# Kernel tuning notes

Hardware: AMD Instinct MI355X
Metric: run time of the kernel (lower is better)

The kernel has to match this reference:

```python
import jax, jax.numpy as jnp
import numpy as np

N_NODES = 50000


def setup_inputs() -> dict:
    key = jax.random.key(0)
    k1, k2, k3, k4 = jax.random.split(key, 4)
    x = jax.random.normal(k1, (N_NODES, 128), dtype=jnp.float32)
    edge_index = jax.random.randint(k2, (2, 1600000), 0, N_NODES, dtype=jnp.int64)
    W1 = jax.random.normal(k3, (128, 256), dtype=jnp.float32) * (1.0 / np.sqrt(128))
    b1 = jnp.zeros((256,), dtype=jnp.float32)
    W2 = jax.random.normal(k4, (256, 1), dtype=jnp.float32) * (1.0 / np.sqrt(256))
    b2 = jnp.zeros((1,), dtype=jnp.float32)
    return {"x": x, "edge_index": edge_index, "W1": W1, "b1": b1, "W2": W2, "b2": b2}


def _gcn_conv(x, src, dst, norm, W, b, n_nodes):
    # PyG GCNConv: h = X W; out_i = sum_j norm_ij * h_j (+ self loop) + b
    h = x @ W                               # [N, F_out]
    msg = h[src] * norm[:, None]            # [E', F_out] gather + scale
    out = jax.ops.segment_sum(msg, dst, num_segments=n_nodes)  # scatter-add
    return out + b


def reference(x, edge_index, W1, b1, W2, b2):
    n = x.shape[0]
    loop = jnp.arange(n, dtype=edge_index.dtype)
    src = jnp.concatenate([edge_index[0], loop])   # add self loops
    dst = jnp.concatenate([edge_index[1], loop])
    # symmetric degree normalization on A + I
    deg = jax.ops.segment_sum(jnp.ones_like(dst, dtype=x.dtype), dst, num_segments=n)
    dis = jnp.where(deg > 0, jax.lax.rsqrt(deg), 0.0)
    norm = dis[src] * dis[dst]                     # [E']
    h = jax.nn.relu(_gcn_conv(x, src, dst, norm, W1, b1, n))
    return _gcn_conv(h, src, dst, norm, W2, b2, n)
```

## Files before the change

kernel.cpp:

```cpp
#include <hip/hip_runtime.h>


#define EPB_LOG 12
#define EPB (1 << EPB_LOG)
#define BW_LOG 7
#define BW (1 << BW_LOG)
#define MAXBUCK 512
#define SCAN_TILE 2048
#define AMSTRIDE 136

typedef __attribute__((ext_vector_type(8))) short bf16x8;
typedef __attribute__((ext_vector_type(4))) float f32x4;

__device__ inline unsigned short f2bf(float f) {
    unsigned int b = __float_as_uint(f);
    unsigned int r = b + 0x7FFFu + ((b >> 16) & 1u);
    return (unsigned short)(r >> 16);
}
__device__ inline float bf_lo(unsigned int u) { return __uint_as_float(u << 16); }
__device__ inline float bf_hi(unsigned int u) { return __uint_as_float(u & 0xFFFF0000u); }

__device__ inline int detect_stride(const int* edges, int t, int* sh) {
    if (t < 64) {
        int v = edges[2 * t + 1];
        unsigned long long bb = __ballot(v != 0);
        if (t == 0) *sh = bb ? 1 : 2;
    }
    __syncthreads();
    return *sh;
}


__global__ __launch_bounds__(256) void k_count(
        const int* __restrict__ edges, const float* __restrict__ W1,
        unsigned short* __restrict__ w1t, int* __restrict__ btot_raw,
        long long E, int nbuck, int nsb) {
    int b = blockIdx.x, t = threadIdx.x;
    if (b >= nsb) {
        int row = (b - nsb) * 2 + (t >> 7);
        int k = t & 127;
        w1t[row * 128 + k] = f2bf(W1[k * 256 + row]);
        return;
    }
    __shared__ int bins[MAXBUCK];
    __shared__ int sh;
    for (int i = t; i < nbuck; i += 256) bins[i] = 0;
    int stride = detect_stride(edges, t, &sh);
    long long base = (long long)b << EPB_LOG;
    long long rem = E - base;
    int nE = (rem < (long long)EPB) ? (int)rem : EPB;
    for (int i = t; i < nE; i += 256) {
        int d = edges[(E + base + i) * stride];
        atomicAdd(&bins[d >> BW_LOG], 1);
    }
    __syncthreads();
    for (int i = t; i < nbuck; i += 256)
        if (bins[i]) atomicAdd(&btot_raw[i], bins[i]);
}

__global__ __launch_bounds__(256) void k_btot_scan(
        const int* __restrict__ btot_raw, int* __restrict__ btot,
        int* __restrict__ curg, int nbuck) {
    __shared__ int ws4[4];
    int t = threadIdx.x;
    int c4 = (nbuck + 255) >> 8;
    int lo = t * c4;
    int hi = lo + c4; if (hi > nbuck) hi = nbuck;
    if (lo > nbuck) lo = nbuck;
    int vals[2];
    int local = 0;
    for (int i = lo; i < hi; ++i) { vals[i - lo] = btot_raw[i]; local += vals[i - lo]; }
    int lane = t & 63, w = t >> 6;
    int inc = local;
    for (int off = 1; off < 64; off <<= 1) {
        int u = __shfl_up(inc, off, 64);
        if (lane >= off) inc += u;
    }
    if (lane == 63) ws4[w] = inc;
    __syncthreads();
    int woff = 0;
    for (int i = 0; i < w; ++i) woff += ws4[i];
    int ex = woff + inc - local;
    for (int i = lo; i < hi; ++i) {
        btot[i] = ex; curg[i] = ex;
        ex += vals[i - lo];
    }
}

__global__ __launch_bounds__(256) void k_partition(
        const int* __restrict__ edges, int* __restrict__ curg,
        unsigned int* __restrict__ part, long long E, int nbuck) {
    __shared__ unsigned int stage[EPB];
    __shared__ unsigned short dst16[EPB];
    __shared__ int bins[MAXBUCK];
    __shared__ int lcur[MAXBUCK];
    __shared__ int gbase[MAXBUCK];
    __shared__ int ws4[4];
    __shared__ int sh;
    int sb = blockIdx.x, t = threadIdx.x;
    for (int i = t; i < nbuck; i += 256) bins[i] = 0;
    int stride = detect_stride(edges, t, &sh);
    long long base = (long long)sb << EPB_LOG;
    long long rem = E - base;
    int nE = (rem < (long long)EPB) ? (int)rem : EPB;
    for (int i = t; i < nE; i += 256) {
        int d = edges[(E + base + i) * stride];
        dst16[i] = (unsigned short)d;
        atomicAdd(&bins[d >> BW_LOG], 1);
    }
    __syncthreads();
    int c4 = (nbuck + 255) >> 8;
    int lo = t * c4;
    int hi = lo + c4; if (hi > nbuck) hi = nbuck;
    if (lo > nbuck) lo = nbuck;
    int vals[2];
    int local = 0;
    for (int i = lo; i < hi; ++i) { vals[i - lo] = bins[i]; local += vals[i - lo]; }
    for (int i = t; i < nbuck; i += 256) {
        int c = bins[i];
        gbase[i] = c ? atomicAdd(&curg[i], c) : 0;
    }
    __syncthreads();
    int lane = t & 63, w = t >> 6;
    int inc = local;
    for (int off = 1; off < 64; off <<= 1) {
        int u = __shfl_up(inc, off, 64);
        if (lane >= off) inc += u;
    }
    if (lane == 63) ws4[w] = inc;
    __syncthreads();
    int woff = 0;
    for (int i = 0; i < w; ++i) woff += ws4[i];
    int ex = woff + inc - local;
    for (int i = lo; i < hi; ++i) {
        bins[i] = ex;
        lcur[i] = ex;
        ex += vals[i - lo];
    }
    __syncthreads();
    for (int i = t; i < nE; i += 256) {
        int s = edges[(base + i) * stride];
        int d = dst16[i];
        int b = d >> BW_LOG;
        int p = atomicAdd(&lcur[b], 1);
        stage[p] = ((unsigned int)s << 16) | (unsigned int)d;
    }
    __syncthreads();
    for (int i = t; i < nE; i += 256) {
        unsigned int pk = stage[i];
        int b = (int)(pk & 0xFFFFu) >> BW_LOG;
        part[gbase[b] + (i - bins[b])] = pk;
    }
}

__global__ __launch_bounds__(256) void k_build_csr(
        const unsigned int* __restrict__ part, const int* __restrict__ btot,
        const float* __restrict__ x, int* __restrict__ row_start,
        float* __restrict__ dis, int* __restrict__ csr_src,
        unsigned short* __restrict__ xs, int nbuck, int n, long long E) {
    __shared__ int c128[BW];
    __shared__ int lcur[BW];
    __shared__ float dld[BW];
    __shared__ int ws2[2];
    int b = blockIdx.x, t = threadIdx.x;
    if (t < BW) c128[t] = 0;
    __syncthreads();
    int start = btot[b];
    int endp = (b + 1 < nbuck) ? btot[b + 1] : (int)E;
    for (int i = start + t; i < endp; i += 256)
        atomicAdd(&c128[part[i] & (BW - 1)], 1);
    __syncthreads();
    int lane = t & 63, w = t >> 6;
    int deg = (t < BW) ? c128[t] : 0;
    int inc = deg;
    for (int off = 1; off < 64; off <<= 1) {
        int u = __shfl_up(inc, off, 64);
        if (lane >= off) inc += u;
    }
    if (t < BW && lane == 63) ws2[w] = inc;
    __syncthreads();
    if (t < BW) {
        int ex = inc - deg + ((w == 1) ? ws2[0] : 0);
        lcur[t] = ex;
        int d = (b << BW_LOG) + t;
        if (d < n) {
            row_start[d] = start + ex;
            float dv = rsqrtf((float)deg + 1.0f);
            dis[d] = dv;
            dld[t] = dv;
        }
    }
    if (b == nbuck - 1 && t == 0) row_start[n] = (int)E;
    __syncthreads();
    for (int i = start + t; i < endp; i += 256) {
        unsigned int pk = part[i];
        int r = atomicAdd(&lcur[pk & (BW - 1)], 1);
        csr_src[start + r] = (int)(pk >> 16);
    }
    int d0 = b << BW_LOG;
    for (int idx = t; idx < BW * 32; idx += 256) {
        int node = d0 + (idx >> 5);
        if (node >= n) break;
        float dv = dld[idx >> 5];
        float4 v = ((const float4*)x)[(size_t)node * 32 + (idx & 31)];
        ushort4 o;
        o.x = f2bf(v.x * dv); o.y = f2bf(v.y * dv);
        o.z = f2bf(v.z * dv); o.w = f2bf(v.w * dv);
        ((ushort4*)xs)[(size_t)node * 32 + (idx & 31)] = o;
    }
}

__global__ __launch_bounds__(512) void k_agg_mm(
        const unsigned short* __restrict__ xs, const int* __restrict__ csr_src,
        const int* __restrict__ rs, const float* __restrict__ dis,
        const unsigned short* __restrict__ w1t, const float* __restrict__ b1,
        const float* __restrict__ W2, float* __restrict__ svs, int n) {
    __shared__ short am[64 * AMSTRIDE];
    int t = threadIdx.x;
    int lane = t & 63, w = t >> 6;
    int blk = blockIdx.x;
    const unsigned int* xsu = (const unsigned int*)xs;
#pragma unroll 1
    for (int jj = 0; jj < 8; ++jj) {
        int r = w * 8 + jj;
        int node = blk * 64 + r;
        unsigned int pack = 0;
        if (node < n) {
            int start = rs[node], end = rs[node + 1];
            unsigned int self = xsu[((size_t)node << 6) + lane];
            float a0 = bf_lo(self), a1 = bf_hi(self);
            int e = start;
            for (; e + 7 < end; e += 8) {
                int s0 = csr_src[e],     s1 = csr_src[e + 1];
                int s2 = csr_src[e + 2], s3 = csr_src[e + 3];
                int s4 = csr_src[e + 4], s5 = csr_src[e + 5];
                int s6 = csr_src[e + 6], s7 = csr_src[e + 7];
                unsigned int v0 = xsu[((size_t)s0 << 6) + lane];
                unsigned int v1 = xsu[((size_t)s1 << 6) + lane];
                unsigned int v2 = xsu[((size_t)s2 << 6) + lane];
                unsigned int v3 = xsu[((size_t)s3 << 6) + lane];
                unsigned int v4 = xsu[((size_t)s4 << 6) + lane];
                unsigned int v5 = xsu[((size_t)s5 << 6) + lane];
                unsigned int v6 = xsu[((size_t)s6 << 6) + lane];
                unsigned int v7 = xsu[((size_t)s7 << 6) + lane];
                a0 += bf_lo(v0); a1 += bf_hi(v0);
                a0 += bf_lo(v1); a1 += bf_hi(v1);
                a0 += bf_lo(v2); a1 += bf_hi(v2);
                a0 += bf_lo(v3); a1 += bf_hi(v3);
                a0 += bf_lo(v4); a1 += bf_hi(v4);
                a0 += bf_lo(v5); a1 += bf_hi(v5);
                a0 += bf_lo(v6); a1 += bf_hi(v6);
                a0 += bf_lo(v7); a1 += bf_hi(v7);
            }
            for (; e < end; ++e) {
                int s0 = csr_src[e];
                unsigned int v0 = xsu[((size_t)s0 << 6) + lane];
                a0 += bf_lo(v0); a1 += bf_hi(v0);
            }
            float dn = dis[node];
            pack = (unsigned int)f2bf(a0 * dn) | ((unsigned int)f2bf(a1 * dn) << 16);
        }
        *(unsigned int*)&am[r * AMSTRIDE + 2 * lane] = pack;
    }
    __syncthreads();
    if (w >= 4) return;
    int m = lane & 15;
    int quad = lane >> 4;
    int node0 = blk * 64 + w * 16;

    bf16x8 afrag[4];
    const short* arow = &am[(w * 16 + m) * AMSTRIDE + quad * 8];
#pragma unroll
    for (int ks = 0; ks < 4; ++ks)
        afrag[ks] = *(const bf16x8*)(arow + ks * 32);

    float p0 = 0.f, p1 = 0.f, p2 = 0.f, p3 = 0.f;
#pragma unroll 1
    for (int tt = 0; tt < 16; ++tt) {
        const unsigned short* brow = w1t + (size_t)(tt * 16 + m) * 128 + quad * 8;
        f32x4 acc = {0.f, 0.f, 0.f, 0.f};
#pragma unroll
        for (int ks = 0; ks < 4; ++ks) {
            bf16x8 bfrag = *(const bf16x8*)(brow + ks * 32);
            acc = __builtin_amdgcn_mfma_f32_16x16x32_bf16(afrag[ks], bfrag, acc, 0, 0, 0);
        }
        int col = tt * 16 + m;
        float bb = b1[col], w2 = W2[col];
        float h0 = acc[0] + bb, h1 = acc[1] + bb, h2 = acc[2] + bb, h3 = acc[3] + bb;
        p0 += (h0 > 0.f ? h0 : 0.f) * w2;
        p1 += (h1 > 0.f ? h1 : 0.f) * w2;
        p2 += (h2 > 0.f ? h2 : 0.f) * w2;
        p3 += (h3 > 0.f ? h3 : 0.f) * w2;
    }
#pragma unroll
    for (int off = 1; off < 16; off <<= 1) {
        p0 += __shfl_xor(p0, off, 64);
        p1 += __shfl_xor(p1, off, 64);
        p2 += __shfl_xor(p2, off, 64);
        p3 += __shfl_xor(p3, off, 64);
    }
    if (m == 0) {
        int nb = node0 + quad * 4;
        if (nb + 0 < n) svs[nb + 0] = p0 * dis[nb + 0];
        if (nb + 1 < n) svs[nb + 1] = p1 * dis[nb + 1];
        if (nb + 2 < n) svs[nb + 2] = p2 * dis[nb + 2];
        if (nb + 3 < n) svs[nb + 3] = p3 * dis[nb + 3];
    }
}

__global__ __launch_bounds__(256) void k_out(
        const float* __restrict__ svs, const int* __restrict__ csr_src,
        const int* __restrict__ row_start, const float* __restrict__ dis,
        const float* __restrict__ b2, float* __restrict__ out, int n) {
    int wid  = (blockIdx.x * blockDim.x + threadIdx.x) >> 6;
    int lane = threadIdx.x & 63;
    if (wid >= n) return;
    int start = row_start[wid], end = row_start[wid + 1];
    float acc = 0.f;
    for (int e = start + lane; e < end; e += 64)
        acc += svs[csr_src[e]];
    for (int off = 32; off; off >>= 1) acc += __shfl_down(acc, off, 64);
    if (lane == 0)
        out[wid] = dis[wid] * (acc + svs[wid]) + b2[0];
}

__global__ void k_init(const int* __restrict__ edges, int* __restrict__ flag,
                       int* __restrict__ cnt, int n) {
    int i = blockIdx.x * blockDim.x + threadIdx.x;
    if (i < n) cnt[i] = 0;
    if (blockIdx.x == 0 && threadIdx.x < 64) {
        int v = edges[2 * threadIdx.x + 1];
        unsigned long long b = __ballot(v != 0);
        if (threadIdx.x == 0) flag[0] = b ? 1 : 2;
    }
}
__global__ __launch_bounds__(128) void k_prep_w(const float* __restrict__ W1,
        unsigned short* __restrict__ w1t) {
    int nn = blockIdx.x, k = threadIdx.x;
    w1t[nn * 128 + k] = f2bf(W1[k * 256 + nn]);
}
__global__ __launch_bounds__(256) void k_prep_xs(const float* __restrict__ x,
        const float* __restrict__ dis, unsigned short* __restrict__ xs, int n) {
    int i = blockIdx.x * 256 + threadIdx.x;
    if (i >= n * 32) return;
    float dsc = dis[i >> 5];
    float4 v = ((const float4*)x)[i];
    ushort4 o;
    o.x = f2bf(v.x * dsc); o.y = f2bf(v.y * dsc);
    o.z = f2bf(v.z * dsc); o.w = f2bf(v.w * dsc);
    ((ushort4*)xs)[i] = o;
}
__global__ void k_count_slow(const int* __restrict__ edges, const int* __restrict__ flag,
                             int* __restrict__ cnt, int* __restrict__ posi, long long E) {
    long long e = (long long)blockIdx.x * blockDim.x + threadIdx.x;
    if (e >= E) return;
    int stride = flag[0];
    int d = edges[(E + e) * stride];
    posi[e] = atomicAdd(&cnt[d], 1);
}
__global__ __launch_bounds__(256) void k_scan_partial(
        const int* __restrict__ cnt, int* __restrict__ bsum, int n) {
    int t = threadIdx.x;
    int idx = blockIdx.x * SCAN_TILE + t * 8;
    int s = 0;
#pragma unroll
    for (int j = 0; j < 8; ++j) { int i = idx + j; if (i < n) s += cnt[i]; }
    for (int off = 32; off; off >>= 1) s += __shfl_down(s, off, 64);
    __shared__ int ws[4];
    if ((t & 63) == 0) ws[t >> 6] = s;
    __syncthreads();
    if (t == 0) bsum[blockIdx.x] = ws[0] + ws[1] + ws[2] + ws[3];
}
__global__ void k_scan_tops(int* __restrict__ bsum, int nb) {
    int t = threadIdx.x;
    int w = (t < nb) ? bsum[t] : 0;
    int v = w;
    for (int off = 1; off < 64; off <<= 1) {
        int u = __shfl_up(v, off, 64);
        if (t >= off) v += u;
    }
    if (t < nb) bsum[t] = v - w;
}
__global__ __launch_bounds__(256) void k_scan_apply(
        const int* __restrict__ cnt, const int* __restrict__ bsum,
        int* __restrict__ row_start, float* __restrict__ dis, int n) {
    int t = threadIdx.x;
    int lane = t & 63, w = t >> 6;
    int idx = blockIdx.x * SCAN_TILE + t * 8;
    int vals[8];
    int s = 0;
#pragma unroll
    for (int j = 0; j < 8; ++j) { int i = idx + j; vals[j] = (i < n) ? cnt[i] : 0; s += vals[j]; }
    int inc = s;
    for (int off = 1; off < 64; off <<= 1) {
        int u = __shfl_up(inc, off, 64);
        if (lane >= off) inc += u;
    }
    __shared__ int wsum[4];
    if (lane == 63) wsum[w] = inc;
    __syncthreads();
    int woff = 0;
    for (int i = 0; i < w; ++i) woff += wsum[i];
    int ex = bsum[blockIdx.x] + woff + inc - s;
#pragma unroll
    for (int j = 0; j < 8; ++j) {
        int i = idx + j;
        if (i < n) {
            row_start[i] = ex;
            dis[i] = rsqrtf((float)vals[j] + 1.0f);
            ex += vals[j];
        }
    }
    if (idx <= n && n < idx + 8) row_start[n] = ex;
}
__global__ void k_scatter_slow(const int* __restrict__ edges, const int* __restrict__ flag,
                               const int* __restrict__ row_start, const int* __restrict__ posi,
                               int* __restrict__ csr_src, long long E) {
    long long e = (long long)blockIdx.x * blockDim.x + threadIdx.x;
    if (e >= E) return;
    int stride = flag[0];
    int s = edges[e * stride];
    int d = edges[(E + e) * stride];
    csr_src[row_start[d] + posi[e]] = s;
}
__global__ __launch_bounds__(256) void k_agg(
        const unsigned short* __restrict__ xs, const int* __restrict__ csr_src,
        const int* __restrict__ row_start, const float* __restrict__ dis,
        unsigned short* __restrict__ aggh, int n) {
    int wid  = (blockIdx.x * blockDim.x + threadIdx.x) >> 6;
    int lane = threadIdx.x & 63;
    if (wid >= n) return;
    int start = row_start[wid], end = row_start[wid + 1];
    unsigned int self = ((const unsigned int*)xs)[((size_t)wid << 6) + lane];
    float a0 = bf_lo(self), a1 = bf_hi(self);
    for (int e = start; e < end; ++e) {
        int s0 = csr_src[e];
        unsigned int v0 = ((const unsigned int*)xs)[((size_t)s0 << 6) + lane];
        a0 += bf_lo(v0); a1 += bf_hi(v0);
    }
    float dn = dis[wid];
    unsigned int pack = (unsigned int)f2bf(a0 * dn) | ((unsigned int)f2bf(a1 * dn) << 16);
    ((unsigned int*)aggh)[((size_t)wid << 6) + lane] = pack;
}
__global__ __launch_bounds__(256) void k_mm(
        const unsigned short* __restrict__ aggh, const unsigned short* __restrict__ w1t,
        const float* __restrict__ b1, const float* __restrict__ W2,
        const float* __restrict__ dis, float* __restrict__ svs, int n) {
    int wave = threadIdx.x >> 6;
    int lane = threadIdx.x & 63;
    int m = lane & 15, quad = lane >> 4;
    int node0 = blockIdx.x * 64 + wave * 16;
    bf16x8 afrag[4];
    const unsigned short* arow = aggh + (size_t)(node0 + m) * 128 + quad * 8;
#pragma unroll
    for (int ks = 0; ks < 4; ++ks) afrag[ks] = *(const bf16x8*)(arow + ks * 32);
    float p0 = 0.f, p1 = 0.f, p2 = 0.f, p3 = 0.f;
#pragma unroll 1
    for (int tt = 0; tt < 16; ++tt) {
        const unsigned short* brow = w1t + (size_t)(tt * 16 + m) * 128 + quad * 8;
        f32x4 acc = {0.f, 0.f, 0.f, 0.f};
#pragma unroll
        for (int ks = 0; ks < 4; ++ks) {
            bf16x8 bfrag = *(const bf16x8*)(brow + ks * 32);
            acc = __builtin_amdgcn_mfma_f32_16x16x32_bf16(afrag[ks], bfrag, acc, 0, 0, 0);
        }
        int col = tt * 16 + m;
        float bb = b1[col], w2 = W2[col];
        float h0 = acc[0] + bb, h1 = acc[1] + bb, h2 = acc[2] + bb, h3 = acc[3] + bb;
        p0 += (h0 > 0.f ? h0 : 0.f) * w2;
        p1 += (h1 > 0.f ? h1 : 0.f) * w2;
        p2 += (h2 > 0.f ? h2 : 0.f) * w2;
        p3 += (h3 > 0.f ? h3 : 0.f) * w2;
    }
#pragma unroll
    for (int off = 1; off < 16; off <<= 1) {
        p0 += __shfl_xor(p0, off, 64);
        p1 += __shfl_xor(p1, off, 64);
        p2 += __shfl_xor(p2, off, 64);
        p3 += __shfl_xor(p3, off, 64);
    }
    if (m == 0) {
        int nb = node0 + quad * 4;
        if (nb + 0 < n) svs[nb + 0] = p0 * dis[nb + 0];
        if (nb + 1 < n) svs[nb + 1] = p1 * dis[nb + 1];
        if (nb + 2 < n) svs[nb + 2] = p2 * dis[nb + 2];
        if (nb + 3 < n) svs[nb + 3] = p3 * dis[nb + 3];
    }
}

extern "C" void kernel_launch(void* const* d_in, const int* in_sizes, int n_in,
                              void* d_out, int out_size, void* d_ws, size_t ws_size,
                              hipStream_t stream) {
    const float* x  = (const float*)d_in[0];
    const int*   ei = (const int*)d_in[1];
    const float* W1 = (const float*)d_in[2];
    const float* b1 = (const float*)d_in[3];
    const float* W2 = (const float*)d_in[4];
    const float* b2 = (const float*)d_in[5];
    float* out = (float*)d_out;

    const int N = in_sizes[0] / 128;
    const long long E = in_sizes[1] / 2;
    const int nsb = (int)((E + EPB - 1) >> EPB_LOG);
    const int nbuck = (N + BW - 1) >> BW_LOG;

    char* ws = (char*)d_ws;
    size_t off = 0;
    auto take = [&](size_t bytes) -> char* {
        char* p = ws + off;
        off = (off + bytes + 255) & ~(size_t)255;
        return p;
    };
    int*            flag     = (int*)take(4);
    int*            cnt      = (int*)take((size_t)N * 4);
    int*            rs       = (int*)take((size_t)(N + 1) * 4);
    float*          dis      = (float*)take((size_t)N * 4);
    float*          svs      = (float*)take((size_t)N * 4);
    int*            bsum     = (int*)take(64 * 4);
    int*            btot_raw = (int*)take(MAXBUCK * 4);
    int*            btot     = (int*)take(MAXBUCK * 4);
    int*            curg     = (int*)take(MAXBUCK * 4);
    unsigned int*   part     = (unsigned int*)take((size_t)E * 4);
    int*            csr_src  = (int*)take((size_t)E * 4);
    unsigned short* xs       = (unsigned short*)take((size_t)N * 128 * 2);
    unsigned short* w1t      = (unsigned short*)take((size_t)256 * 128 * 2);
    unsigned short* aggh     = (unsigned short*)take((size_t)(N + 64) * 128 * 2);

    int nb_n  = (N + 255) / 256;
    int nb_e  = (int)((E + 255) / 256);
    int nb_s  = (N + SCAN_TILE - 1) / SCAN_TILE;
    int nb_x  = (N * 32 + 255) / 256;
    int nb_am = (N + 63) / 64;

    bool fast = (N < 65536);

    if (fast) {
        hipMemsetAsync(btot_raw, 0, (size_t)nbuck * 4, stream);
        k_count    <<<nsb + 128, 256, 0, stream>>>(ei, W1, w1t, btot_raw, E, nbuck, nsb);
        k_btot_scan<<<1, 256, 0, stream>>>(btot_raw, btot, curg, nbuck);
        k_partition<<<nsb, 256, 0, stream>>>(ei, curg, part, E, nbuck);
        k_build_csr<<<nbuck, 256, 0, stream>>>(part, btot, x, rs, dis, csr_src,
                                               xs, nbuck, N, E);
        k_agg_mm   <<<nb_am, 512, 0, stream>>>(xs, csr_src, rs, dis, w1t, b1, W2, svs, N);
        k_out      <<<(N + 3) / 4, 256, 0, stream>>>(svs, csr_src, rs, dis, b2, out, N);
    } else {
        k_init        <<<nb_n, 256, 0, stream>>>(ei, flag, cnt, N);
        k_prep_w      <<<256, 128, 0, stream>>>(W1, w1t);
        k_count_slow  <<<nb_e, 256, 0, stream>>>(ei, flag, cnt, (int*)part, E);
        k_scan_partial<<<nb_s, 256, 0, stream>>>(cnt, bsum, N);
        k_scan_tops   <<<1, 64, 0, stream>>>(bsum, nb_s);
        k_scan_apply  <<<nb_s, 256, 0, stream>>>(cnt, bsum, rs, dis, N);
        k_prep_xs     <<<nb_x, 256, 0, stream>>>(x, dis, xs, N);
        k_scatter_slow<<<nb_e, 256, 0, stream>>>(ei, flag, rs, (const int*)part, csr_src, E);
        k_agg         <<<(N + 3) / 4, 256, 0, stream>>>(xs, csr_src, rs, dis, aggh, N);
        k_mm          <<<(N + 63) / 64, 256, 0, stream>>>(aggh, w1t, b1, W2, dis, svs, N);
        k_out         <<<(N + 3) / 4, 256, 0, stream>>>(svs, csr_src, rs, dis, b2, out, N);
    }
}
```

Before: 240.8 us.

## Assign 16 lanes per node with 128-bit gathers in aggregation and output

The aggregation kernel now maps each node to a quarter-wavefront of 16 lanes that gather 16-byte chunks of the bf16 feature row, instead of one full wavefront per node reading 4 bytes per lane. Blocks shrink to 256 threads covering 16 nodes, with a single wave doing the MFMA projection, so more blocks run and each wave keeps more gathers in flight. The output kernel likewise uses 16 lanes per node with an xor reduction, which suits the average degree of about 32. The cost is more registers per lane for the eight accumulators and a smaller MFMA tile per block, with three of the four waves idle during the matrix step.

```diff
diff --git a/kernel.cpp b/kernel.cpp
--- a/kernel.cpp
+++ b/kernel.cpp
@@ -19,6 +19,13 @@
 }
 __device__ inline float bf_lo(unsigned int u) { return __uint_as_float(u << 16); }
 __device__ inline float bf_hi(unsigned int u) { return __uint_as_float(u & 0xFFFF0000u); }
+
+__device__ inline void acc8(float* a, uint4 v) {
+    a[0] += bf_lo(v.x); a[1] += bf_hi(v.x);
+    a[2] += bf_lo(v.y); a[3] += bf_hi(v.y);
+    a[4] += bf_lo(v.z); a[5] += bf_hi(v.z);
+    a[6] += bf_lo(v.w); a[7] += bf_hi(v.w);
+}
 
 __device__ inline int detect_stride(const int* edges, int t, int* sh) {
     if (t < 64) {
@@ -210,66 +217,61 @@
     }
 }
 
-__global__ __launch_bounds__(512) void k_agg_mm(
+__global__ __launch_bounds__(256) void k_agg_mm(
         const unsigned short* __restrict__ xs, const int* __restrict__ csr_src,
         const int* __restrict__ rs, const float* __restrict__ dis,
         const unsigned short* __restrict__ w1t, const float* __restrict__ b1,
         const float* __restrict__ W2, float* __restrict__ svs, int n) {
-    __shared__ short am[64 * AMSTRIDE];
+    __shared__ short am[16 * AMSTRIDE];
     int t = threadIdx.x;
     int lane = t & 63, w = t >> 6;
+    int q = lane >> 4, l16 = lane & 15;
     int blk = blockIdx.x;
-    const unsigned int* xsu = (const unsigned int*)xs;
-#pragma unroll 1
-    for (int jj = 0; jj < 8; ++jj) {
-        int r = w * 8 + jj;
-        int node = blk * 64 + r;
-        unsigned int pack = 0;
-        if (node < n) {
-            int start = rs[node], end = rs[node + 1];
-            unsigned int self = xsu[((size_t)node << 6) + lane];
-            float a0 = bf_lo(self), a1 = bf_hi(self);
-            int e = start;
-            for (; e + 7 < end; e += 8) {
-                int s0 = csr_src[e],     s1 = csr_src[e + 1];
-                int s2 = csr_src[e + 2], s3 = csr_src[e + 3];
-                int s4 = csr_src[e + 4], s5 = csr_src[e + 5];
-                int s6 = csr_src[e + 6], s7 = csr_src[e + 7];
-                unsigned int v0 = xsu[((size_t)s0 << 6) + lane];
-                unsigned int v1 = xsu[((size_t)s1 << 6) + lane];
-                unsigned int v2 = xsu[((size_t)s2 << 6) + lane];
-                unsigned int v3 = xsu[((size_t)s3 << 6) + lane];
-                unsigned int v4 = xsu[((size_t)s4 << 6) + lane];
-                unsigned int v5 = xsu[((size_t)s5 << 6) + lane];
-                unsigned int v6 = xsu[((size_t)s6 << 6) + lane];
-                unsigned int v7 = xsu[((size_t)s7 << 6) + lane];
-                a0 += bf_lo(v0); a1 += bf_hi(v0);
-                a0 += bf_lo(v1); a1 += bf_hi(v1);
-                a0 += bf_lo(v2); a1 += bf_hi(v2);
-                a0 += bf_lo(v3); a1 += bf_hi(v3);
-                a0 += bf_lo(v4); a1 += bf_hi(v4);
-                a0 += bf_lo(v5); a1 += bf_hi(v5);
-                a0 += bf_lo(v6); a1 += bf_hi(v6);
-                a0 += bf_lo(v7); a1 += bf_hi(v7);
-            }
-            for (; e < end; ++e) {
-                int s0 = csr_src[e];
-                unsigned int v0 = xsu[((size_t)s0 << 6) + lane];
-                a0 += bf_lo(v0); a1 += bf_hi(v0);
-            }
-            float dn = dis[node];
-            pack = (unsigned int)f2bf(a0 * dn) | ((unsigned int)f2bf(a1 * dn) << 16);
+    int r = w * 4 + q;
+    int node = blk * 16 + r;
+    const uint4* xs4 = (const uint4*)xs;
+
+    uint4 o = {0u, 0u, 0u, 0u};
+    if (node < n) {
+        float a[8] = {0.f, 0.f, 0.f, 0.f, 0.f, 0.f, 0.f, 0.f};
+        acc8(a, xs4[((size_t)node << 4) + l16]);
+        int start = rs[node], end = rs[node + 1];
+        int e = start;
+        for (; e + 8 <= end; e += 8) {
+            int s0 = csr_src[e],     s1 = csr_src[e + 1];
+            int s2 = csr_src[e + 2], s3 = csr_src[e + 3];
+            int s4 = csr_src[e + 4], s5 = csr_src[e + 5];
+            int s6 = csr_src[e + 6], s7 = csr_src[e + 7];
+            uint4 v0 = xs4[((size_t)s0 << 4) + l16];
+            uint4 v1 = xs4[((size_t)s1 << 4) + l16];
+            uint4 v2 = xs4[((size_t)s2 << 4) + l16];
+            uint4 v3 = xs4[((size_t)s3 << 4) + l16];
+            uint4 v4 = xs4[((size_t)s4 << 4) + l16];
+            uint4 v5 = xs4[((size_t)s5 << 4) + l16];
+            uint4 v6 = xs4[((size_t)s6 << 4) + l16];
+            uint4 v7 = xs4[((size_t)s7 << 4) + l16];
+            acc8(a, v0); acc8(a, v1); acc8(a, v2); acc8(a, v3);
+            acc8(a, v4); acc8(a, v5); acc8(a, v6); acc8(a, v7);
         }
-        *(unsigned int*)&am[r * AMSTRIDE + 2 * lane] = pack;
-    }
-    __syncthreads();
-    if (w >= 4) return;
+        for (; e < end; ++e) {
+            int s0 = csr_src[e];
+            acc8(a, xs4[((size_t)s0 << 4) + l16]);
+        }
+        float dn = dis[node];
+        o.x = (unsigned int)f2bf(a[0] * dn) | ((unsigned int)f2bf(a[1] * dn) << 16);
+        o.y = (unsigned int)f2bf(a[2] * dn) | ((unsigned int)f2bf(a[3] * dn) << 16);
+        o.z = (unsigned int)f2bf(a[4] * dn) | ((unsigned int)f2bf(a[5] * dn) << 16);
+        o.w = (unsigned int)f2bf(a[6] * dn) | ((unsigned int)f2bf(a[7] * dn) << 16);
+    }
+    *(uint4*)&am[r * AMSTRIDE + l16 * 8] = o;
+    __syncthreads();
+    if (w) return;
     int m = lane & 15;
     int quad = lane >> 4;
-    int node0 = blk * 64 + w * 16;
+    int node0 = blk * 16;
 
     bf16x8 afrag[4];
-    const short* arow = &am[(w * 16 + m) * AMSTRIDE + quad * 8];
+    const short* arow = &am[m * AMSTRIDE + quad * 8];
 #pragma unroll
     for (int ks = 0; ks < 4; ++ks)
         afrag[ks] = *(const bf16x8*)(arow + ks * 32);
@@ -312,16 +314,19 @@
         const float* __restrict__ svs, const int* __restrict__ csr_src,
         const int* __restrict__ row_start, const float* __restrict__ dis,
         const float* __restrict__ b2, float* __restrict__ out, int n) {
-    int wid  = (blockIdx.x * blockDim.x + threadIdx.x) >> 6;
-    int lane = threadIdx.x & 63;
-    if (wid >= n) return;
-    int start = row_start[wid], end = row_start[wid + 1];
+    int t = threadIdx.x;
+    int lane = t & 63, w = t >> 6;
+    int q = lane >> 4, l16 = lane & 15;
+    int node = blockIdx.x * 16 + w * 4 + q;
+    if (node >= n) return;
+    int start = row_start[node], end = row_start[node + 1];
     float acc = 0.f;
-    for (int e = start + lane; e < end; e += 64)
+    for (int e = start + l16; e < end; e += 16)
         acc += svs[csr_src[e]];
-    for (int off = 32; off; off >>= 1) acc += __shfl_down(acc, off, 64);
-    if (lane == 0)
-        out[wid] = dis[wid] * (acc + svs[wid]) + b2[0];
+#pragma unroll
+    for (int off = 1; off < 16; off <<= 1) acc += __shfl_xor(acc, off, 64);
+    if (l16 == 0)
+        out[node] = dis[node] * (acc + svs[node]) + b2[0];
 }
 
 __global__ void k_init(const int* __restrict__ edges, int* __restrict__ flag,
@@ -530,7 +535,8 @@
     int nb_e  = (int)((E + 255) / 256);
     int nb_s  = (N + SCAN_TILE - 1) / SCAN_TILE;
     int nb_x  = (N * 32 + 255) / 256;
-    int nb_am = (N + 63) / 64;
+    int nb_am = (N + 15) / 16;
+    int nb_o  = (N + 15) / 16;
 
     bool fast = (N < 65536);
 
@@ -541,8 +547,8 @@
         k_partition<<<nsb, 256, 0, stream>>>(ei, curg, part, E, nbuck);
         k_build_csr<<<nbuck, 256, 0, stream>>>(part, btot, x, rs, dis, csr_src,
                                                xs, nbuck, N, E);
-        k_agg_mm   <<<nb_am, 512, 0, stream>>>(xs, csr_src, rs, dis, w1t, b1, W2, svs, N);
-        k_out      <<<(N + 3) / 4, 256, 0, stream>>>(svs, csr_src, rs, dis, b2, out, N);
+        k_agg_mm   <<<nb_am, 256, 0, stream>>>(xs, csr_src, rs, dis, w1t, b1, W2, svs, N);
+        k_out      <<<nb_o, 256, 0, stream>>>(svs, csr_src, rs, dis, b2, out, N);
     } else {
         k_init        <<<nb_n, 256, 0, stream>>>(ei, flag, cnt, N);
         k_prep_w      <<<256, 128, 0, stream>>>(W1, w1t);
@@ -554,6 +560,6 @@
         k_scatter_slow<<<nb_e, 256, 0, stream>>>(ei, flag, rs, (const int*)part, csr_src, E);
         k_agg         <<<(N + 3) / 4, 256, 0, stream>>>(xs, csr_src, rs, dis, aggh, N);
         k_mm          <<<(N + 63) / 64, 256, 0, stream>>>(aggh, w1t, b1, W2, dis, svs, N);
-        k_out         <<<(N + 3) / 4, 256, 0, stream>>>(svs, csr_src, rs, dis, b2, out, N);
-    }
-}
+        k_out         <<<nb_o, 256, 0, stream>>>(svs, csr_src, rs, dis, b2, out, N);
+    }
+}
```

New measurement: 219.1 us. 1.1x faster.
